# Kernel tuning notes

Hardware: AMD Instinct MI355X
Metric: run time of the kernel (lower is better)

## Reference

```python
import jax, jax.numpy as jnp
import numpy as np

N_NODES = 100000
N_EDGES = 1600000
DIM = 64          # num_features == hidden_dim
N_LAYERS = 5
N_GRAPHS = 1024
EMB = DIM * N_LAYERS  # 320
BN_EPS = 1e-5


def setup_inputs() -> dict:
    key = jax.random.key(0)
    ks = jax.random.split(key, 16)
    s = 0.05
    return {
        "x": jax.random.normal(ks[0], (N_NODES, DIM), dtype=jnp.float32),
        "edge_index": jax.random.randint(ks[1], (2, N_EDGES), 0, N_NODES, dtype=jnp.int32),
        "edge_weight": jax.random.uniform(ks[2], (N_EDGES,), dtype=jnp.float32),
        "batch": jnp.sort(jax.random.randint(ks[3], (N_NODES,), 0, N_GRAPHS, dtype=jnp.int32)),
        # stacked per-layer GIN MLP params: nn = Linear(d,d) -> ReLU -> Linear(d,d)
        "W1s": jax.random.normal(ks[4], (N_LAYERS, DIM, DIM), dtype=jnp.float32) * s,
        "b1s": jnp.zeros((N_LAYERS, DIM), dtype=jnp.float32),
        "W2s": jax.random.normal(ks[5], (N_LAYERS, DIM, DIM), dtype=jnp.float32) * s,
        "b2s": jnp.zeros((N_LAYERS, DIM), dtype=jnp.float32),
        # BatchNorm1d affine params (init: weight=1, bias=0)
        "gammas": jnp.ones((N_LAYERS, DIM), dtype=jnp.float32),
        "betas": jnp.zeros((N_LAYERS, DIM), dtype=jnp.float32),
        # projection head: Linear(EMB,EMB) -> ReLU -> Linear(EMB,EMB)
        "pW1": jax.random.normal(ks[6], (EMB, EMB), dtype=jnp.float32) * s,
        "pb1": jnp.zeros((EMB,), dtype=jnp.float32),
        "pW2": jax.random.normal(ks[7], (EMB, EMB), dtype=jnp.float32) * s,
        "pb2": jnp.zeros((EMB,), dtype=jnp.float32),
    }


def _encoder(x, src, dst, edge_weight, batch,
             W1s, b1s, W2s, b2s, gammas, betas):
    h = x
    pooled = []
    for i in range(N_LAYERS):
        # WGINConv (eps=0): h_out = nn(h + sum_{j->i} w_ij * h_j)
        msg = jax.ops.segment_sum(h[src] * edge_weight[:, None], dst,
                                  num_segments=N_NODES)  # [N, D]
        z = h + msg
        z = jnp.maximum(z @ W1s[i] + b1s[i], 0.0) @ W2s[i] + b2s[i]
        h = jnp.maximum(z, 0.0)  # F.relu after conv
        # BatchNorm1d (training mode: batch stats over nodes, biased var)
        mean = jnp.mean(h, axis=0)
        var = jnp.var(h, axis=0)
        h = (h - mean) * jax.lax.rsqrt(var + BN_EPS) * gammas[i] + betas[i]
        pooled.append(h)
    # global_mean_pool per layer, then concat along feature dim
    counts = jax.ops.segment_sum(jnp.ones((N_NODES,), h.dtype), batch,
                                 num_segments=N_GRAPHS)
    counts = jnp.maximum(counts, 1.0)[:, None]
    xpool = [jax.ops.segment_sum(h, batch, num_segments=N_GRAPHS) / counts
             for h in pooled]
    return jnp.concatenate(xpool, axis=1)  # [G, L*D]


def reference(x, edge_index, edge_weight, batch,
              W1s, b1s, W2s, b2s, gammas, betas,
              pW1, pb1, pW2, pb2):
    src, dst = edge_index[0], edge_index[1]
    y = _encoder(x, src, dst, edge_weight, batch,
                 W1s, b1s, W2s, b2s, gammas, betas)
    # proj_head: Linear -> ReLU -> Linear
    y = jnp.maximum(y @ pW1 + pb1, 0.0) @ pW2 + pb2
    return y
```

## Files before the change

### kernel.cpp

```cpp
#include <hip/hip_runtime.h>

#define NN 100000
#define NE 1600000
#define D 64
#define NL 5
#define NG 1024
#define EMBD 320
#define BN_EPS 1e-5f
#define SCAN_NB ((NN + 255) / 256)
#define GIN_NB ((NN + 63) / 64)

__device__ __forceinline__ unsigned short bf16rne(float f) {
  unsigned u = __float_as_uint(f);
  unsigned r = u + 0x7FFFu + ((u >> 16) & 1u);
  return (unsigned short)(r >> 16);
}
__device__ __forceinline__ float bflo(int v) {
  return __uint_as_float(((unsigned)v) << 16);
}
__device__ __forceinline__ float bfhi(int v) {
  return __uint_as_float(((unsigned)v) & 0xFFFF0000u);
}

__global__ __launch_bounds__(256) void k_cvt(const float* __restrict__ in,
                                             unsigned short* __restrict__ outb) {
  int i = blockIdx.x * 256 + threadIdx.x;
  if (i >= NN * 16) return;
  float4 v = ((const float4*)in)[i];
  ushort4 o;
  o.x = bf16rne(v.x); o.y = bf16rne(v.y); o.z = bf16rne(v.z); o.w = bf16rne(v.w);
  ((ushort4*)outb)[i] = o;
}

__global__ __launch_bounds__(256) void k_gbound(const int* __restrict__ batch,
                                                int* __restrict__ gstart) {
  int i = blockIdx.x * 256 + threadIdx.x;
  if (i >= NN) return;
  int b = batch[i];
  int bp = (i == 0) ? -1 : batch[i - 1];
  for (int g = bp + 1; g <= b; ++g) gstart[g] = i;
  if (i == NN - 1) {
    for (int g = b + 1; g <= NG; ++g) gstart[g] = NN;
  }
}

__global__ __launch_bounds__(256) void k_hist(const int* __restrict__ dst,
                                              int* __restrict__ deg) {
  int e = blockIdx.x * 256 + threadIdx.x;
  if (e < NE) atomicAdd(&deg[dst[e]], 1);
}

__global__ __launch_bounds__(256) void k_scan1(const int* __restrict__ deg,
                                               int* __restrict__ bsums) {
  __shared__ int sh[256];
  int i = blockIdx.x * 256 + threadIdx.x;
  sh[threadIdx.x] = (i < NN) ? deg[i] : 0;
  __syncthreads();
  for (int off = 128; off > 0; off >>= 1) {
    if (threadIdx.x < off) sh[threadIdx.x] += sh[threadIdx.x + off];
    __syncthreads();
  }
  if (threadIdx.x == 0) bsums[blockIdx.x] = sh[0];
}

__global__ __launch_bounds__(512) void k_scan2(int* __restrict__ bsums) {
  __shared__ int sh[512];
  int t = threadIdx.x;
  int v = (t < SCAN_NB) ? bsums[t] : 0;
  sh[t] = v;
  __syncthreads();
  for (int off = 1; off < 512; off <<= 1) {
    int u = (t >= off) ? sh[t - off] : 0;
    __syncthreads();
    sh[t] += u;
    __syncthreads();
  }
  if (t < SCAN_NB) bsums[t] = sh[t] - v;
}

__global__ __launch_bounds__(256) void k_scan3(int* __restrict__ row_ptr,
                                               int* __restrict__ cursor,
                                               const int* __restrict__ bsums) {
  __shared__ int sh[256];
  int t = threadIdx.x;
  int i = blockIdx.x * 256 + t;
  int v = (i < NN) ? row_ptr[i] : 0;
  sh[t] = v;
  __syncthreads();
  for (int off = 1; off < 256; off <<= 1) {
    int u = (t >= off) ? sh[t - off] : 0;
    __syncthreads();
    sh[t] += u;
    __syncthreads();
  }
  int excl = sh[t] - v + bsums[blockIdx.x];
  if (i < NN) {
    row_ptr[i] = excl;
    cursor[i] = excl;
    if (i == NN - 1) row_ptr[NN] = excl + v;
  }
}

__global__ __launch_bounds__(256) void k_fill(const int* __restrict__ src,
                                              const int* __restrict__ dst,
                                              const float* __restrict__ w,
                                              int* __restrict__ cursor,
                                              int2* __restrict__ epair) {
  int e = blockIdx.x * 256 + threadIdx.x;
  if (e >= NE) return;
  int slot = atomicAdd(&cursor[dst[e]], 1);
  int2 p;
  p.x = src[e];
  p.y = __float_as_int(w[e]);
  epair[slot] = p;
}

#define ACC8(CA, CB, WE)                                                      \
  a0.x = fmaf(bflo(CA.x), WE, a0.x); a0.y = fmaf(bfhi(CA.x), WE, a0.y);       \
  a0.z = fmaf(bflo(CA.y), WE, a0.z); a0.w = fmaf(bfhi(CA.y), WE, a0.w);       \
  a1.x = fmaf(bflo(CA.z), WE, a1.x); a1.y = fmaf(bfhi(CA.z), WE, a1.y);       \
  a1.z = fmaf(bflo(CA.w), WE, a1.z); a1.w = fmaf(bfhi(CA.w), WE, a1.w);       \
  a2.x = fmaf(bflo(CB.x), WE, a2.x); a2.y = fmaf(bfhi(CB.x), WE, a2.y);       \
  a2.z = fmaf(bflo(CB.y), WE, a2.z); a2.w = fmaf(bfhi(CB.y), WE, a2.w);       \
  a3.x = fmaf(bflo(CB.z), WE, a3.x); a3.y = fmaf(bfhi(CB.z), WE, a3.y);       \
  a3.z = fmaf(bflo(CB.w), WE, a3.z); a3.w = fmaf(bfhi(CB.w), WE, a3.w);

__global__ __launch_bounds__(256, 6) void k_gin(const float* __restrict__ x0,
                                                const unsigned short* __restrict__ hbf,
                                                unsigned short* __restrict__ gbf,
                                                const int* __restrict__ row_ptr,
                                                const int2* __restrict__ epair,
                                                const float* __restrict__ W1,
                                                const float* __restrict__ b1,
                                                const float* __restrict__ W2,
                                                const float* __restrict__ b2,
                                                const float* __restrict__ statsP,
                                                const float* __restrict__ gammaP,
                                                const float* __restrict__ betaP,
                                                int first,
                                                float* __restrict__ statsL) {
  __shared__ float zin[64 * 65];
  __shared__ float sW[32 * 64];
  __shared__ float sb[64];
  __shared__ float wsumS[64];
  __shared__ float scA[64], sbA[64];
  const int t = threadIdx.x;
  const int nb = blockIdx.x * 64;
  const int nr = t >> 4, fc = t & 15;

  for (int i = t; i < 2048; i += 256) sW[i] = W1[i];
  if (t < 64) {
    sb[t] = b1[t];
    if (!first) {
      float m = statsP[t] * (1.f / NN);
      float v = fmaxf(statsP[64 + t] * (1.f / NN) - m * m, 0.f);
      float sc = gammaP[t] * rsqrtf(v + BN_EPS);
      scA[t] = sc;
      sbA[t] = betaP[t] - m * sc;
    }
  }

  {
    const int nl = t >> 2;
    const int q = t & 3;
    const int n = nb + nl;
    float4 a0 = {0.f, 0.f, 0.f, 0.f}, a1 = a0, a2 = a0, a3 = a0;
    float wsum = 0.f;
    if (n < NN) {
      const int beg = row_ptr[n], end = row_ptr[n + 1];
      int i = beg;
      for (; i + 2 <= end; i += 2) {
        long long e0 = __builtin_nontemporal_load((const long long*)(epair + i));
        long long e1 = __builtin_nontemporal_load((const long long*)(epair + i + 1));
        int s0 = (int)(e0 & 0xFFFFFFFFll);
        float w0 = __int_as_float((int)(e0 >> 32));
        int s1 = (int)(e1 & 0xFFFFFFFFll);
        float w1 = __int_as_float((int)(e1 >> 32));
        const int4* p0 = (const int4*)(hbf + (size_t)s0 * D);
        const int4* p1 = (const int4*)(hbf + (size_t)s1 * D);
        int4 r0a = p0[2 * q], r0b = p0[2 * q + 1];
        int4 r1a = p1[2 * q], r1b = p1[2 * q + 1];
        ACC8(r0a, r0b, w0)
        wsum += w0;
        ACC8(r1a, r1b, w1)
        wsum += w1;
      }
      for (; i < end; ++i) {
        long long e0 = __builtin_nontemporal_load((const long long*)(epair + i));
        int s0 = (int)(e0 & 0xFFFFFFFFll);
        float w0 = __int_as_float((int)(e0 >> 32));
        const int4* p0 = (const int4*)(hbf + (size_t)s0 * D);
        int4 r0a = p0[2 * q], r0b = p0[2 * q + 1];
        ACC8(r0a, r0b, w0)
        wsum += w0;
      }
      if (first) {
        const float4* own = (const float4*)(x0 + (size_t)n * D) + q * 4;
        float4 o0 = own[0], o1 = own[1], o2 = own[2], o3 = own[3];
        a0.x += o0.x; a0.y += o0.y; a0.z += o0.z; a0.w += o0.w;
        a1.x += o1.x; a1.y += o1.y; a1.z += o1.z; a1.w += o1.w;
        a2.x += o2.x; a2.y += o2.y; a2.z += o2.z; a2.w += o2.w;
        a3.x += o3.x; a3.y += o3.y; a3.z += o3.z; a3.w += o3.w;
      } else {
        const int4* hp = (const int4*)(hbf + (size_t)n * D);
        int4 c0 = hp[2 * q], c1 = hp[2 * q + 1];
        a0.x += bflo(c0.x); a0.y += bfhi(c0.x);
        a0.z += bflo(c0.y); a0.w += bfhi(c0.y);
        a1.x += bflo(c0.z); a1.y += bfhi(c0.z);
        a1.z += bflo(c0.w); a1.w += bfhi(c0.w);
        a2.x += bflo(c1.x); a2.y += bfhi(c1.x);
        a2.z += bflo(c1.y); a2.w += bfhi(c1.y);
        a3.x += bflo(c1.z); a3.y += bfhi(c1.z);
        a3.z += bflo(c1.w); a3.w += bfhi(c1.w);
      }
    }
    float* zr = &zin[nl * 65 + q * 16];
    *(float4*)(zr + 0) = a0;
    *(float4*)(zr + 4) = a1;
    *(float4*)(zr + 8) = a2;
    *(float4*)(zr + 12) = a3;
    if (q == 0) wsumS[nl] = wsum;
  }
  __syncthreads();

  if (!first) {
#pragma unroll
    for (int pass = 0; pass < 4; ++pass) {
      int idx = pass * 1024 + t * 4;
      int r = idx >> 6, c = idx & 63;
      float wp1 = 1.f + wsumS[r];
      float4 z = *(float4*)&zin[r * 65 + c];
      z.x = fmaf(z.x, scA[c + 0], sbA[c + 0] * wp1);
      z.y = fmaf(z.y, scA[c + 1], sbA[c + 1] * wp1);
      z.z = fmaf(z.z, scA[c + 2], sbA[c + 2] * wp1);
      z.w = fmaf(z.w, scA[c + 3], sbA[c + 3] * wp1);
      *(float4*)&zin[r * 65 + c] = z;
    }
    __syncthreads();
  }

#define GEMM_HALF(ACC, KBASE)                                                 \
  _Pragma("unroll 2") for (int kc = 0; kc < 8; ++kc) {                        \
    float4 zv[4], wv[4];                                                      \
    _Pragma("unroll") for (int i = 0; i < 4; ++i)                             \
        zv[i] = *(float4*)&zin[(nr * 4 + i) * 65 + ((KBASE) + kc) * 4];       \
    _Pragma("unroll") for (int kk = 0; kk < 4; ++kk)                          \
        wv[kk] = *(float4*)&sW[(kc * 4 + kk) * 64 + fc * 4];                  \
    _Pragma("unroll") for (int i = 0; i < 4; ++i) {                           \
      ACC[i].x = fmaf(zv[i].x, wv[0].x, ACC[i].x);                            \
      ACC[i].y = fmaf(zv[i].x, wv[0].y, ACC[i].y);                            \
      ACC[i].z = fmaf(zv[i].x, wv[0].z, ACC[i].z);                            \
      ACC[i].w = fmaf(zv[i].x, wv[0].w, ACC[i].w);                            \
      ACC[i].x = fmaf(zv[i].y, wv[1].x, ACC[i].x);                            \
      ACC[i].y = fmaf(zv[i].y, wv[1].y, ACC[i].y);                            \
      ACC[i].z = fmaf(zv[i].y, wv[1].z, ACC[i].z);                            \
      ACC[i].w = fmaf(zv[i].y, wv[1].w, ACC[i].w);                            \
      ACC[i].x = fmaf(zv[i].z, wv[2].x, ACC[i].x);                            \
      ACC[i].y = fmaf(zv[i].z, wv[2].y, ACC[i].y);                            \
      ACC[i].z = fmaf(zv[i].z, wv[2].z, ACC[i].z);                            \
      ACC[i].w = fmaf(zv[i].z, wv[2].w, ACC[i].w);                            \
      ACC[i].x = fmaf(zv[i].w, wv[3].x, ACC[i].x);                            \
      ACC[i].y = fmaf(zv[i].w, wv[3].y, ACC[i].y);                            \
      ACC[i].z = fmaf(zv[i].w, wv[3].z, ACC[i].z);                            \
      ACC[i].w = fmaf(zv[i].w, wv[3].w, ACC[i].w);                            \
    }                                                                         \
  }

#define RELU4(ACC)                                                            \
  _Pragma("unroll") for (int i = 0; i < 4; ++i) {                             \
    ACC[i].x = fmaxf(ACC[i].x, 0.f);                                          \
    ACC[i].y = fmaxf(ACC[i].y, 0.f);                                          \
    ACC[i].z = fmaxf(ACC[i].z, 0.f);                                          \
    ACC[i].w = fmaxf(ACC[i].w, 0.f);                                          \
  }

  float4 acc[4];
  {
    float4 bias = *(float4*)&sb[fc * 4];
#pragma unroll
    for (int i = 0; i < 4; ++i) acc[i] = bias;
  }
  GEMM_HALF(acc, 0)
  __syncthreads();
  for (int i = t; i < 2048; i += 256) sW[i] = W1[2048 + i];
  __syncthreads();
  GEMM_HALF(acc, 8)
  RELU4(acc)
  __syncthreads();

#pragma unroll
  for (int i = 0; i < 4; ++i) *(float4*)&zin[(nr * 4 + i) * 65 + fc * 4] = acc[i];
  for (int i = t; i < 2048; i += 256) sW[i] = W2[i];
  if (t < 64) sb[t] = b2[t];
  __syncthreads();

  float4 acc2[4];
  {
    float4 bias = *(float4*)&sb[fc * 4];
#pragma unroll
    for (int i = 0; i < 4; ++i) acc2[i] = bias;
  }
  GEMM_HALF(acc2, 0)
  __syncthreads();
  for (int i = t; i < 2048; i += 256) sW[i] = W2[2048 + i];
  __syncthreads();
  GEMM_HALF(acc2, 8)
  RELU4(acc2)

  float4 s4 = {0.f, 0.f, 0.f, 0.f}, q4 = {0.f, 0.f, 0.f, 0.f};
#pragma unroll
  for (int i = 0; i < 4; ++i) {
    int n = nb + nr * 4 + i;
    if (n < NN) {
      ushort4 ob;
      ob.x = bf16rne(acc2[i].x);
      ob.y = bf16rne(acc2[i].y);
      ob.z = bf16rne(acc2[i].z);
      ob.w = bf16rne(acc2[i].w);
      *(ushort4*)(gbf + (size_t)n * D + fc * 4) = ob;
      s4.x += acc2[i].x; s4.y += acc2[i].y; s4.z += acc2[i].z; s4.w += acc2[i].w;
      q4.x = fmaf(acc2[i].x, acc2[i].x, q4.x);
      q4.y = fmaf(acc2[i].y, acc2[i].y, q4.y);
      q4.z = fmaf(acc2[i].z, acc2[i].z, q4.z);
      q4.w = fmaf(acc2[i].w, acc2[i].w, q4.w);
    }
  }
#pragma unroll
  for (int m = 16; m <= 32; m <<= 1) {
    s4.x += __shfl_xor(s4.x, m, 64); s4.y += __shfl_xor(s4.y, m, 64);
    s4.z += __shfl_xor(s4.z, m, 64); s4.w += __shfl_xor(s4.w, m, 64);
    q4.x += __shfl_xor(q4.x, m, 64); q4.y += __shfl_xor(q4.y, m, 64);
    q4.z += __shfl_xor(q4.z, m, 64); q4.w += __shfl_xor(q4.w, m, 64);
  }
  __syncthreads();
  int wv_ = t >> 6;
  if ((t & 63) < 16) {
    *(float4*)&zin[wv_ * 64 + fc * 4] = s4;
    *(float4*)&zin[256 + wv_ * 64 + fc * 4] = q4;
  }
  __syncthreads();
  if (t < 64) {
    float S = zin[t] + zin[64 + t] + zin[128 + t] + zin[192 + t];
    float Q = zin[256 + t] + zin[320 + t] + zin[384 + t] + zin[448 + t];
    unsafeAtomicAdd(&statsL[t], S);
    unsafeAtomicAdd(&statsL[64 + t], Q);
  }
#undef GEMM_HALF
#undef RELU4
}

__global__ __launch_bounds__(256) void k_poolraw(const unsigned short* __restrict__ gbf,
                                                 const int* __restrict__ gstart,
                                                 float* __restrict__ pooledraw,
                                                 int layer) {
  __shared__ float4 sh4[256];
  int g = blockIdx.x;
  int beg = gstart[g], end = gstart[g + 1];
  int p = threadIdx.x & 15, r = threadIdx.x >> 4;
  float4 s = {0.f, 0.f, 0.f, 0.f};
  for (int n = beg + r; n < end; n += 16) {
    int2 c = ((const int2*)(gbf + (size_t)n * D))[p];
    s.x += bflo(c.x); s.y += bfhi(c.x);
    s.z += bflo(c.y); s.w += bfhi(c.y);
  }
  sh4[threadIdx.x] = s;
  __syncthreads();
  if (threadIdx.x < 16) {
    float4 tot = {0.f, 0.f, 0.f, 0.f};
#pragma unroll
    for (int j = 0; j < 16; ++j) {
      float4 u = sh4[j * 16 + threadIdx.x];
      tot.x += u.x; tot.y += u.y; tot.z += u.z; tot.w += u.w;
    }
    int cnt = end - beg;
    float inv = 1.0f / (float)(cnt > 1 ? cnt : 1);
    float4 o = {tot.x * inv, tot.y * inv, tot.z * inv, tot.w * inv};
    ((float4*)(pooledraw + (size_t)g * EMBD + layer * D))[threadIdx.x] = o;
  }
}

__global__ __launch_bounds__(EMBD) void k_proj(const float* __restrict__ pooledraw,
                                               const float* __restrict__ stats,
                                               const float* __restrict__ gammas,
                                               const float* __restrict__ betas,
                                               const float* __restrict__ pW1,
                                               const float* __restrict__ pb1,
                                               const float* __restrict__ pW2,
                                               const float* __restrict__ pb2,
                                               float* __restrict__ out) {
  __shared__ float row[EMBD];
  __shared__ float y1[EMBD];
  int g = blockIdx.x, j = threadIdx.x;
  {
    int L = j >> 6, f = j & 63;
    float m = stats[L * 128 + f] * (1.f / NN);
    float v = fmaxf(stats[L * 128 + 64 + f] * (1.f / NN) - m * m, 0.f);
    float sc = gammas[L * D + f] * rsqrtf(v + BN_EPS);
    float sb = betas[L * D + f] - m * sc;
    row[j] = fmaf(pooledraw[(size_t)g * EMBD + j], sc, sb);
  }
  __syncthreads();
  float acc = pb1[j];
#pragma unroll 4
  for (int k = 0; k < EMBD; ++k) acc = fmaf(row[k], pW1[(size_t)k * EMBD + j], acc);
  y1[j] = fmaxf(acc, 0.f);
  __syncthreads();
  acc = pb2[j];
#pragma unroll 4
  for (int k = 0; k < EMBD; ++k) acc = fmaf(y1[k], pW2[(size_t)k * EMBD + j], acc);
  out[(size_t)g * EMBD + j] = acc;
}

extern "C" void kernel_launch(void* const* d_in, const int* in_sizes, int n_in,
                              void* d_out, int out_size, void* d_ws, size_t ws_size,
                              hipStream_t stream) {
  const float* x = (const float*)d_in[0];
  const int* ei = (const int*)d_in[1];
  const float* ew = (const float*)d_in[2];
  const int* batch = (const int*)d_in[3];
  const float* W1s = (const float*)d_in[4];
  const float* b1s = (const float*)d_in[5];
  const float* W2s = (const float*)d_in[6];
  const float* b2s = (const float*)d_in[7];
  const float* gammas = (const float*)d_in[8];
  const float* betas = (const float*)d_in[9];
  const float* pW1 = (const float*)d_in[10];
  const float* pb1 = (const float*)d_in[11];
  const float* pW2 = (const float*)d_in[12];
  const float* pb2 = (const float*)d_in[13];
  const int* srcv = ei;
  const int* dstv = ei + NE;

  char* ws = (char*)d_ws;
  float* stats = (float*)ws;
  float* pooledraw = stats + NL * 128;
  int* gstart = (int*)(pooledraw + (size_t)NG * EMBD);
  int* row_ptr = gstart + NG + 1;
  int* cursor = row_ptr + NN + 1;
  int2* epair = (int2*)(cursor + NN);
  int* bsums = (int*)(epair + NE);
  unsigned short* hbfA = (unsigned short*)(bsums + SCAN_NB);
  unsigned short* hbfB = hbfA + (size_t)NN * D;

  hipMemsetAsync(row_ptr, 0, (NN + 1) * sizeof(int), stream);
  hipMemsetAsync(stats, 0, NL * 128 * sizeof(float), stream);
  k_hist<<<(NE + 255) / 256, 256, 0, stream>>>(dstv, row_ptr);
  k_scan1<<<SCAN_NB, 256, 0, stream>>>(row_ptr, bsums);
  k_scan2<<<1, 512, 0, stream>>>(bsums);
  k_scan3<<<SCAN_NB, 256, 0, stream>>>(row_ptr, cursor, bsums);
  k_fill<<<(NE + 255) / 256, 256, 0, stream>>>(srcv, dstv, ew, cursor, epair);
  k_gbound<<<SCAN_NB, 256, 0, stream>>>(batch, gstart);
  k_cvt<<<(NN * 16 + 255) / 256, 256, 0, stream>>>(x, hbfA);

  unsigned short* bfin = hbfA;
  unsigned short* bfout = hbfB;
  for (int L = 0; L < NL; ++L) {
    k_gin<<<GIN_NB, 256, 0, stream>>>(x, bfin, bfout, row_ptr, epair,
                                      W1s + L * D * D, b1s + L * D,
                                      W2s + L * D * D, b2s + L * D,
                                      stats + (L > 0 ? (L - 1) * 128 : 0),
                                      gammas + (L > 0 ? (L - 1) * D : 0),
                                      betas + (L > 0 ? (L - 1) * D : 0),
                                      L == 0 ? 1 : 0,
                                      stats + L * 128);
    k_poolraw<<<NG, 256, 0, stream>>>(bfout, gstart, pooledraw, L);
    unsigned short* tmpb = bfin;
    bfin = bfout;
    bfout = tmpb;
  }
  k_proj<<<NG, EMBD, 0, stream>>>(pooledraw, stats, gammas, betas,
                                  pW1, pb1, pW2, pb2, (float*)d_out);
}
```

Baseline: 830.4 us.

## Bucket CSR edges by source range within each destination row

Builds the CSR with 7 sub-buckets per destination node keyed by source index >> 14, so each node's edges are loosely sorted by source. This aims to improve L2 locality of the bf16 feature gathers in the GIN aggregation across the five layers. It costs a histogram, scan and cursor array seven times larger, plus a rewritten single-block scan that handles about 2.7k block sums.

```diff
diff --git a/kernel.cpp b/kernel.cpp
--- a/kernel.cpp
+++ b/kernel.cpp
@@ -9,6 +9,9 @@
 #define BN_EPS 1e-5f
 #define SCAN_NB ((NN + 255) / 256)
 #define GIN_NB ((NN + 63) / 64)
+#define SRCB 7
+#define M2 (NN * SRCB)
+#define SCAN2_NB ((M2 + 255) / 256)
 
 __device__ __forceinline__ unsigned short bf16rne(float f) {
   unsigned u = __float_as_uint(f);
@@ -44,17 +47,21 @@
   }
 }
 
-__global__ __launch_bounds__(256) void k_hist(const int* __restrict__ dst,
+__global__ __launch_bounds__(256) void k_hist(const int* __restrict__ src,
+                                              const int* __restrict__ dst,
                                               int* __restrict__ deg) {
   int e = blockIdx.x * 256 + threadIdx.x;
-  if (e < NE) atomicAdd(&deg[dst[e]], 1);
+  if (e >= NE) return;
+  int s = __builtin_nontemporal_load(src + e);
+  int d = __builtin_nontemporal_load(dst + e);
+  atomicAdd(&deg[d * SRCB + (s >> 14)], 1);
 }
 
 __global__ __launch_bounds__(256) void k_scan1(const int* __restrict__ deg,
                                                int* __restrict__ bsums) {
   __shared__ int sh[256];
   int i = blockIdx.x * 256 + threadIdx.x;
-  sh[threadIdx.x] = (i < NN) ? deg[i] : 0;
+  sh[threadIdx.x] = (i < M2) ? deg[i] : 0;
   __syncthreads();
   for (int off = 128; off > 0; off >>= 1) {
     if (threadIdx.x < off) sh[threadIdx.x] += sh[threadIdx.x + off];
@@ -63,19 +70,31 @@
   if (threadIdx.x == 0) bsums[blockIdx.x] = sh[0];
 }
 
-__global__ __launch_bounds__(512) void k_scan2(int* __restrict__ bsums) {
-  __shared__ int sh[512];
+__global__ __launch_bounds__(1024) void k_scan2(int* __restrict__ bsums) {
+  __shared__ int sh[1024];
   int t = threadIdx.x;
-  int v = (t < SCAN_NB) ? bsums[t] : 0;
-  sh[t] = v;
-  __syncthreads();
-  for (int off = 1; off < 512; off <<= 1) {
+  int loc[3];
+  int s = 0;
+#pragma unroll
+  for (int i = 0; i < 3; ++i) {
+    int idx = t * 3 + i;
+    loc[i] = s;
+    if (idx < SCAN2_NB) s += bsums[idx];
+  }
+  sh[t] = s;
+  __syncthreads();
+  for (int off = 1; off < 1024; off <<= 1) {
     int u = (t >= off) ? sh[t - off] : 0;
     __syncthreads();
     sh[t] += u;
     __syncthreads();
   }
-  if (t < SCAN_NB) bsums[t] = sh[t] - v;
+  int base = sh[t] - s;
+#pragma unroll
+  for (int i = 0; i < 3; ++i) {
+    int idx = t * 3 + i;
+    if (idx < SCAN2_NB) bsums[idx] = base + loc[i];
+  }
 }
 
 __global__ __launch_bounds__(256) void k_scan3(int* __restrict__ row_ptr,
@@ -84,7 +103,7 @@
   __shared__ int sh[256];
   int t = threadIdx.x;
   int i = blockIdx.x * 256 + t;
-  int v = (i < NN) ? row_ptr[i] : 0;
+  int v = (i < M2) ? row_ptr[i] : 0;
   sh[t] = v;
   __syncthreads();
   for (int off = 1; off < 256; off <<= 1) {
@@ -94,10 +113,10 @@
     __syncthreads();
   }
   int excl = sh[t] - v + bsums[blockIdx.x];
-  if (i < NN) {
+  if (i < M2) {
     row_ptr[i] = excl;
     cursor[i] = excl;
-    if (i == NN - 1) row_ptr[NN] = excl + v;
+    if (i == M2 - 1) row_ptr[M2] = excl + v;
   }
 }
 
@@ -108,10 +127,13 @@
                                               int2* __restrict__ epair) {
   int e = blockIdx.x * 256 + threadIdx.x;
   if (e >= NE) return;
-  int slot = atomicAdd(&cursor[dst[e]], 1);
+  int s = __builtin_nontemporal_load(src + e);
+  int d = __builtin_nontemporal_load(dst + e);
+  float we = __builtin_nontemporal_load(w + e);
+  int slot = atomicAdd(&cursor[d * SRCB + (s >> 14)], 1);
   int2 p;
-  p.x = src[e];
-  p.y = __float_as_int(w[e]);
+  p.x = s;
+  p.y = __float_as_int(we);
   epair[slot] = p;
 }
 
@@ -167,7 +189,7 @@
     float4 a0 = {0.f, 0.f, 0.f, 0.f}, a1 = a0, a2 = a0, a3 = a0;
     float wsum = 0.f;
     if (n < NN) {
-      const int beg = row_ptr[n], end = row_ptr[n + 1];
+      const int beg = row_ptr[n * SRCB], end = row_ptr[n * SRCB + SRCB];
       int i = beg;
       for (; i + 2 <= end; i += 2) {
         long long e0 = __builtin_nontemporal_load((const long long*)(epair + i));
@@ -436,18 +458,18 @@
   float* pooledraw = stats + NL * 128;
   int* gstart = (int*)(pooledraw + (size_t)NG * EMBD);
   int* row_ptr = gstart + NG + 1;
-  int* cursor = row_ptr + NN + 1;
-  int2* epair = (int2*)(cursor + NN);
+  int* cursor = row_ptr + M2 + 1;
+  int2* epair = (int2*)(cursor + M2);
   int* bsums = (int*)(epair + NE);
-  unsigned short* hbfA = (unsigned short*)(bsums + SCAN_NB);
+  unsigned short* hbfA = (unsigned short*)(bsums + SCAN2_NB);
   unsigned short* hbfB = hbfA + (size_t)NN * D;
 
-  hipMemsetAsync(row_ptr, 0, (NN + 1) * sizeof(int), stream);
+  hipMemsetAsync(row_ptr, 0, (M2 + 1) * sizeof(int), stream);
   hipMemsetAsync(stats, 0, NL * 128 * sizeof(float), stream);
-  k_hist<<<(NE + 255) / 256, 256, 0, stream>>>(dstv, row_ptr);
-  k_scan1<<<SCAN_NB, 256, 0, stream>>>(row_ptr, bsums);
-  k_scan2<<<1, 512, 0, stream>>>(bsums);
-  k_scan3<<<SCAN_NB, 256, 0, stream>>>(row_ptr, cursor, bsums);
+  k_hist<<<(NE + 255) / 256, 256, 0, stream>>>(srcv, dstv, row_ptr);
+  k_scan1<<<SCAN2_NB, 256, 0, stream>>>(row_ptr, bsums);
+  k_scan2<<<1, 1024, 0, stream>>>(bsums);
+  k_scan3<<<SCAN2_NB, 256, 0, stream>>>(row_ptr, cursor, bsums);
   k_fill<<<(NE + 255) / 256, 256, 0, stream>>>(srcv, dstv, ew, cursor, epair);
   k_gbound<<<SCAN_NB, 256, 0, stream>>>(batch, gstart);
   k_cvt<<<(NN * 16 + 255) / 256, 256, 0, stream>>>(x, hbfA);
```

Result: faster. 805.1 us (-3.1%).
